# Kernel optimization log

Hardware: AMD Instinct MI355X
Metric: run time of the kernel (lower is better)

Reference implementation:

```python
import jax, jax.numpy as jnp
import numpy as np

N = 50000       # nodes
E = 800000      # edges
D_IN = 128
D_OUT = 128
K = 3           # num_stacks
T = 2           # num_layers


def setup_inputs() -> dict:
    key = jax.random.key(0)
    ks = jax.random.split(key, 10)
    feats = jax.random.normal(ks[0], (N, D_IN), dtype=jnp.float32)
    src = jax.random.randint(ks[1], (E,), 0, N, dtype=jnp.int32)
    dst = jax.random.randint(ks[2], (E,), 0, N, dtype=jnp.int32)
    s = 0.05
    w0 = jax.random.normal(ks[3], (K, D_IN, D_OUT), dtype=jnp.float32) * s
    b0 = jax.random.normal(ks[4], (K, D_OUT), dtype=jnp.float32) * s
    w = jax.random.normal(ks[5], (K, D_OUT, D_OUT), dtype=jnp.float32) * s
    bw = jax.random.normal(ks[6], (K, D_OUT), dtype=jnp.float32) * s
    v = jax.random.normal(ks[7], (K, D_IN, D_OUT), dtype=jnp.float32) * s
    bv = jax.random.normal(ks[8], (K, D_OUT), dtype=jnp.float32) * s
    return {"feats": feats, "src": src, "dst": dst,
            "w0": w0, "b0": b0, "w": w, "bw": bw, "v": v, "bv": bv}


def _propagate(h, src, dst, norm):
    # symmetric degree-normalized SpMM: D^{-1/2} A D^{-1/2} h
    h = h * norm                                   # [N, d]
    agg = jax.ops.segment_sum(h[src], dst, num_segments=N)  # gather + scatter-add
    return agg * norm


def reference(feats, src, dst, w0, b0, w, bw, v, bv):
    ones = jnp.ones((E,), dtype=feats.dtype)
    deg = jnp.clip(jax.ops.segment_sum(ones, dst, num_segments=N), 1.0)
    norm = (deg ** -0.5)[:, None]                  # [N, 1]

    out = jnp.zeros((N, D_OUT), dtype=feats.dtype)
    for k in range(K):
        h = feats
        for t in range(T):
            h = _propagate(h, src, dst, norm)
            if t == 0:
                h = h @ w0[k] + b0[k]
            else:
                h = h @ w[k] + bw[k]
            h = h + (feats @ v[k] + bv[k])         # dropout is identity (p=0, eval)
            h = jax.nn.relu(h)
        out = out + h
    return out / K
```

## Files before the change

kernel.cpp:

```cpp
#include <hip/hip_runtime.h>

#define N_NODES 50000
#define N_EDGES 800000
#define D 128
#define PLANE ((size_t)N_NODES * D)
#define NCHUNK ((N_NODES + 255) / 256)

typedef float f32x4 __attribute__((ext_vector_type(4)));
typedef float f32x2 __attribute__((ext_vector_type(2)));
typedef short bf16x8 __attribute__((ext_vector_type(8)));

__device__ __forceinline__ unsigned short f2bf(float x) {
  unsigned int u = __float_as_uint(x);
  u += 0x7FFFu + ((u >> 16) & 1u);
  return (unsigned short)(u >> 16);
}
__device__ __forceinline__ unsigned char f32_to_fp8(float x) {
  int p = __builtin_amdgcn_cvt_pk_fp8_f32(x, x, 0, false);
  return (unsigned char)(p & 0xFF);
}


__global__ __launch_bounds__(256) void scan_local(const int* __restrict__ cnt,
                                                  int* __restrict__ local,
                                                  int* __restrict__ partial,
                                                  int* __restrict__ bcnt) {
  __shared__ int s[256];
  __shared__ int hist[64];
  int t = threadIdx.x;
  if (t < 64) hist[t] = 0;
  int i = blockIdx.x * 256 + t;
  int v = (i < N_NODES) ? cnt[i] : 0;
  s[t] = v;
  __syncthreads();
  if (i < N_NODES) atomicAdd(&hist[v < 63 ? v : 63], 1);
  for (int off = 1; off < 256; off <<= 1) {
    int tmp = (t >= off) ? s[t - off] : 0;
    __syncthreads();
    s[t] += tmp;
    __syncthreads();
  }
  if (i < N_NODES) local[i] = s[t] - v;
  if (t == 255) partial[blockIdx.x] = s[255];
  if (t < 64) atomicAdd(&bcnt[t], hist[t]);
}

__global__ __launch_bounds__(256) void scan_chunks(const int* __restrict__ partial,
                                                   int* __restrict__ chunk_off,
                                                   int* __restrict__ rowptr,
                                                   const int* __restrict__ bcnt,
                                                   int* __restrict__ gcur) {
  __shared__ int s[256];
  __shared__ int sb[64];
  __shared__ int sbb[64];
  int t = threadIdx.x;
  int v = (t < NCHUNK) ? partial[t] : 0;
  s[t] = v;
  if (t < 64) sb[t] = bcnt[t];
  __syncthreads();
  if (t == 0) {
    int run = 0;
    for (int q = 0; q < 64; ++q) { sbb[q] = run; run += sb[q]; }
  }
  for (int off = 1; off < 256; off <<= 1) {
    int tmp = (t >= off) ? s[t - off] : 0;
    __syncthreads();
    s[t] += tmp;
    __syncthreads();
  }
  if (t < NCHUNK) chunk_off[t] = s[t] - v;
  if (t == 255) rowptr[N_NODES] = s[255];
  if (t < 64) gcur[t] = sbb[t];
}

__global__ __launch_bounds__(256) void finalize_rows(const int* __restrict__ cnt,
                                                     const int* __restrict__ local,
                                                     const int* __restrict__ chunk_off,
                                                     int* __restrict__ rowptr,
                                                     int* __restrict__ cursor,
                                                     float* __restrict__ norm,
                                                     int* __restrict__ gcur,
                                                     int* __restrict__ perm) {
  __shared__ int hcnt[64];
  __shared__ int hbase[64];
  int t = threadIdx.x;
  if (t < 64) hcnt[t] = 0;
  __syncthreads();
  int i = blockIdx.x * 256 + t;
  int b = 0;
  if (i < N_NODES) {
    int r = local[i] + chunk_off[blockIdx.x];
    rowptr[i] = r;
    cursor[i] = r;
    int d = cnt[i];
    b = d < 63 ? d : 63;
    atomicAdd(&hcnt[b], 1);
    if (d < 1) d = 1;
    norm[i] = rsqrtf((float)d);
  }
  __syncthreads();
  if (t < 64) {
    hbase[t] = atomicAdd(&gcur[t], hcnt[t]);
    hcnt[t] = 0;
  }
  __syncthreads();
  if (i < N_NODES) {
    int lp = atomicAdd(&hcnt[b], 1);
    perm[hbase[b] + lp] = i;
  }
}


#define CONV_THREADS ((int)(PLANE / 4))
#define WT_THREADS (2 * 3 * 128 * 256)
#define PREP_TOTAL (CONV_THREADS + WT_THREADS + N_EDGES)

__global__ __launch_bounds__(256) void prep_all(const float* __restrict__ feats,
                                                const float* __restrict__ w0,
                                                const float* __restrict__ w,
                                                const float* __restrict__ v,
                                                const int* __restrict__ dst,
                                                unsigned short* __restrict__ feats_bf,
                                                unsigned short* __restrict__ bt_h1,
                                                unsigned short* __restrict__ bt_out,
                                                int* __restrict__ cnt) {
  int idx = blockIdx.x * 256 + threadIdx.x;
  if (idx < CONV_THREADS) {
    float4 x = ((const float4*)feats)[idx];
    ushort4 o;
    o.x = f2bf(x.x);
    o.y = f2bf(x.y);
    o.z = f2bf(x.z);
    o.w = f2bf(x.w);
    ((ushort4*)feats_bf)[idx] = o;
    return;
  }
  idx -= CONV_THREADS;
  if (idx < WT_THREADS) {
    int buf = idx / 98304;
    int rem = idx - buf * 98304;
    int stack = rem / 32768;
    int rem2 = rem & 32767;
    int n = rem2 >> 8;
    int k = rem2 & 255;
    const float* srcm;
    int kk;
    if (k < 128) {
      srcm = (buf == 0) ? w0 : w;
      kk = k;
    } else {
      srcm = v;
      kk = k - 128;
    }
    float val = srcm[(size_t)stack * 16384 + (size_t)kk * 128 + n];
    unsigned short* dstb = (buf == 0) ? bt_h1 : bt_out;
    dstb[(size_t)stack * 32768 + (size_t)n * 256 + k] = f2bf(val);
    return;
  }
  idx -= WT_THREADS;
  if (idx < N_EDGES) atomicAdd(&cnt[dst[idx]], 1);
}

__global__ __launch_bounds__(256) void csr_fp8(const int* __restrict__ src,
                                               const int* __restrict__ dst,
                                               int* __restrict__ cursor,
                                               int* __restrict__ col,
                                               const float* __restrict__ feats,
                                               const float* __restrict__ norm,
                                               unsigned char* __restrict__ feats_fp8) {
  int idx = blockIdx.x * 256 + threadIdx.x;
  if (idx < CONV_THREADS) {
    float4 x = ((const float4*)feats)[idx];
    float nv = norm[idx >> 5];
    int p = __builtin_amdgcn_cvt_pk_fp8_f32(x.x * nv, x.y * nv, 0, false);
    p = __builtin_amdgcn_cvt_pk_fp8_f32(x.z * nv, x.w * nv, p, true);
    ((int*)feats_fp8)[idx] = p;
    return;
  }
  idx -= CONV_THREADS;
  if (idx < N_EDGES) {
    int pos = atomicAdd(&cursor[dst[idx]], 1);
    col[pos] = src[idx];
  }
}


template <int NK, int STRIDE>
__global__ __launch_bounds__(256) void spmm_rows(const unsigned char* __restrict__ h,
                                                 const float* __restrict__ norm,
                                                 const int* __restrict__ rowptr,
                                                 const int* __restrict__ col,
                                                 const int* __restrict__ perm,
                                                 unsigned short* __restrict__ out) {
  int gi = blockIdx.x * 32 + (threadIdx.x >> 3);
  if (gi >= N_NODES) return;
  int l = threadIdx.x & 7;
  int row = perm[gi];
  int beg = rowptr[row], end = rowptr[row + 1];

  f32x2 acc[NK][8];
#pragma unroll
  for (int m = 0; m < NK; ++m)
#pragma unroll
    for (int j = 0; j < 8; ++j) acc[m][j] = (f32x2)(0.f);

#pragma unroll 2
  for (int e = beg; e < end; ++e) {
    int s = col[e];
    const unsigned char* hp = h + (size_t)s * STRIDE + l * 16;
#pragma unroll
    for (int m = 0; m < NK; ++m) {
      int4 p = *(const int4*)(hp + m * 128);
      acc[m][0] += __builtin_amdgcn_cvt_pk_f32_fp8(p.x, false);
      acc[m][1] += __builtin_amdgcn_cvt_pk_f32_fp8(p.x, true);
      acc[m][2] += __builtin_amdgcn_cvt_pk_f32_fp8(p.y, false);
      acc[m][3] += __builtin_amdgcn_cvt_pk_f32_fp8(p.y, true);
      acc[m][4] += __builtin_amdgcn_cvt_pk_f32_fp8(p.z, false);
      acc[m][5] += __builtin_amdgcn_cvt_pk_f32_fp8(p.z, true);
      acc[m][6] += __builtin_amdgcn_cvt_pk_f32_fp8(p.w, false);
      acc[m][7] += __builtin_amdgcn_cvt_pk_f32_fp8(p.w, true);
    }
  }

  float nd = norm[row];
#pragma unroll
  for (int m = 0; m < NK; ++m) {
    bf16x8 o0, o1;
#pragma unroll
    for (int j = 0; j < 4; ++j) {
      o0[2 * j] = (short)f2bf(acc[m][j].x * nd);
      o0[2 * j + 1] = (short)f2bf(acc[m][j].y * nd);
      o1[2 * j] = (short)f2bf(acc[m][j + 4].x * nd);
      o1[2 * j + 1] = (short)f2bf(acc[m][j + 4].y * nd);
    }
    unsigned short* op = out + (size_t)m * PLANE + (size_t)row * D + l * 16;
    *(bf16x8*)op = o0;
    *(bf16x8*)(op + 8) = o1;
  }
}


__device__ __forceinline__ void stage_B64(unsigned short (*Bs)[256],
                                          const unsigned short* __restrict__ Btg,
                                          int nh, int tid) {
#pragma unroll
  for (int i = 0; i < 8; ++i) {
    int t = tid + i * 256;
    int n = t >> 5;
    int kc = t & 31;
    int kcs = kc ^ (n & 31);
    *(bf16x8*)&Bs[n][kcs * 8] = *(const bf16x8*)(Btg + (size_t)(nh + n) * 256 + kc * 8);
  }
}

__device__ __forceinline__ bf16x8 read_B64(const unsigned short (*Bs)[256], int n,
                                           int chunk) {
  return *(const bf16x8*)&Bs[n][(chunk ^ (n & 31)) * 8];
}

__global__ __launch_bounds__(256) void gemm_h1_fused(
    const unsigned short* __restrict__ P,
    const unsigned short* __restrict__ feats_bf,
    const unsigned short* __restrict__ Bt,
    const float* __restrict__ b0, const float* __restrict__ bv,
    const float* __restrict__ norm,
    unsigned char* __restrict__ h1_fp8) {
  __shared__ unsigned short Bs[64][256];
  int nh = blockIdx.y * 64;

  int tid = threadIdx.x;
  int lane = tid & 63;
  int wv = tid >> 6;
  int ln15 = lane & 15;
  int g = lane >> 4;

  int m0 = blockIdx.x * 128 + wv * 32;
  int r0 = m0 + ln15;
  int r1 = m0 + 16 + ln15;
  if (r0 >= N_NODES) r0 = N_NODES - 1;
  if (r1 >= N_NODES) r1 = N_NODES - 1;

  bf16x8 a0[8], a1[8];
#pragma unroll
  for (int s = 0; s < 4; ++s) {
    a0[s] = *(const bf16x8*)(P + (size_t)r0 * 128 + g * 8 + s * 32);
    a1[s] = *(const bf16x8*)(P + (size_t)r1 * 128 + g * 8 + s * 32);
    a0[s + 4] = *(const bf16x8*)(feats_bf + (size_t)r0 * 128 + g * 8 + s * 32);
    a1[s + 4] = *(const bf16x8*)(feats_bf + (size_t)r1 * 128 + g * 8 + s * 32);
  }

  float nA[4], nB[4];
#pragma unroll
  for (int r = 0; r < 4; ++r) {
    int mA = m0 + g * 4 + r;
    int mB = m0 + 16 + g * 4 + r;
    nA[r] = (mA < N_NODES) ? norm[mA] : 0.f;
    nB[r] = (mB < N_NODES) ? norm[mB] : 0.f;
  }

  for (int stk = 0; stk < 3; ++stk) {
    if (stk) __syncthreads();
    stage_B64(Bs, Bt + (size_t)stk * 32768, nh, tid);
    __syncthreads();

    f32x4 acc0[4], acc1[4];
#pragma unroll
    for (int nt = 0; nt < 4; ++nt) { acc0[nt] = (f32x4)(0.f); acc1[nt] = (f32x4)(0.f); }

#pragma unroll
    for (int s = 0; s < 8; ++s) {
#pragma unroll
      for (int nt = 0; nt < 4; ++nt) {
        bf16x8 bfr = read_B64(Bs, nt * 16 + ln15, s * 4 + g);
        acc0[nt] = __builtin_amdgcn_mfma_f32_16x16x32_bf16(a0[s], bfr, acc0[nt], 0, 0, 0);
        acc1[nt] = __builtin_amdgcn_mfma_f32_16x16x32_bf16(a1[s], bfr, acc1[nt], 0, 0, 0);
      }
    }

#pragma unroll
    for (int nt = 0; nt < 4; ++nt) {
      int colj = nh + nt * 16 + ln15;
      float bsum = b0[stk * 128 + colj] + bv[stk * 128 + colj];
#pragma unroll
      for (int r = 0; r < 4; ++r) {
        int mA = m0 + g * 4 + r;
        int mB = m0 + 16 + g * 4 + r;
        if (mA < N_NODES) {
          float x = acc0[nt][r] + bsum;
          x = x > 0.f ? x : 0.f;
          h1_fp8[(size_t)mA * 384 + stk * 128 + colj] = f32_to_fp8(x * nA[r]);
        }
        if (mB < N_NODES) {
          float x = acc1[nt][r] + bsum;
          x = x > 0.f ? x : 0.f;
          h1_fp8[(size_t)mB * 384 + stk * 128 + colj] = f32_to_fp8(x * nB[r]);
        }
      }
    }
  }
}

__global__ __launch_bounds__(256) void gemm_out_fused(
    const unsigned short* __restrict__ agg,
    const unsigned short* __restrict__ feats_bf,
    const unsigned short* __restrict__ Bt,
    const float* __restrict__ bwp, const float* __restrict__ bvp,
    float* __restrict__ outp) {
  __shared__ unsigned short Bs[64][256];
  int nh = blockIdx.y * 64;

  int tid = threadIdx.x;
  int lane = tid & 63;
  int wv = tid >> 6;
  int ln15 = lane & 15;
  int g = lane >> 4;

  int m0 = blockIdx.x * 128 + wv * 32;
  int r0 = m0 + ln15;
  int r1 = m0 + 16 + ln15;
  if (r0 >= N_NODES) r0 = N_NODES - 1;
  if (r1 >= N_NODES) r1 = N_NODES - 1;

  bf16x8 f0[4], f1[4];
#pragma unroll
  for (int s = 0; s < 4; ++s) {
    f0[s] = *(const bf16x8*)(feats_bf + (size_t)r0 * 128 + g * 8 + s * 32);
    f1[s] = *(const bf16x8*)(feats_bf + (size_t)r1 * 128 + g * 8 + s * 32);
  }

  f32x4 sum0[4], sum1[4];
#pragma unroll
  for (int nt = 0; nt < 4; ++nt) { sum0[nt] = (f32x4)(0.f); sum1[nt] = (f32x4)(0.f); }

  for (int stk = 0; stk < 3; ++stk) {
    if (stk) __syncthreads();
    stage_B64(Bs, Bt + (size_t)stk * 32768, nh, tid);
    __syncthreads();

    const unsigned short* A1 = agg + (size_t)stk * PLANE;
    bf16x8 g0[4], g1[4];
#pragma unroll
    for (int s = 0; s < 4; ++s) {
      g0[s] = *(const bf16x8*)(A1 + (size_t)r0 * 128 + g * 8 + s * 32);
      g1[s] = *(const bf16x8*)(A1 + (size_t)r1 * 128 + g * 8 + s * 32);
    }

    f32x4 acc0[4], acc1[4];
#pragma unroll
    for (int nt = 0; nt < 4; ++nt) { acc0[nt] = (f32x4)(0.f); acc1[nt] = (f32x4)(0.f); }

#pragma unroll
    for (int s = 0; s < 8; ++s) {
      bf16x8 af0 = (s < 4) ? g0[s & 3] : f0[s & 3];
      bf16x8 af1 = (s < 4) ? g1[s & 3] : f1[s & 3];
#pragma unroll
      for (int nt = 0; nt < 4; ++nt) {
        bf16x8 bfr = read_B64(Bs, nt * 16 + ln15, s * 4 + g);
        acc0[nt] = __builtin_amdgcn_mfma_f32_16x16x32_bf16(af0, bfr, acc0[nt], 0, 0, 0);
        acc1[nt] = __builtin_amdgcn_mfma_f32_16x16x32_bf16(af1, bfr, acc1[nt], 0, 0, 0);
      }
    }

#pragma unroll
    for (int nt = 0; nt < 4; ++nt) {
      int colj = nh + nt * 16 + ln15;
      float bsum = bwp[stk * 128 + colj] + bvp[stk * 128 + colj];
#pragma unroll
      for (int r = 0; r < 4; ++r) {
        float x0 = acc0[nt][r] + bsum;
        float x1 = acc1[nt][r] + bsum;
        sum0[nt][r] += (x0 > 0.f ? x0 : 0.f);
        sum1[nt][r] += (x1 > 0.f ? x1 : 0.f);
      }
    }
  }

  const float sc = 1.0f / 3.0f;
#pragma unroll
  for (int nt = 0; nt < 4; ++nt) {
    int colj = nh + nt * 16 + ln15;
#pragma unroll
    for (int r = 0; r < 4; ++r) {
      int mA = m0 + g * 4 + r;
      int mB = m0 + 16 + g * 4 + r;
      if (mA < N_NODES) outp[(size_t)mA * 128 + colj] = sum0[nt][r] * sc;
      if (mB < N_NODES) outp[(size_t)mB * 128 + colj] = sum1[nt][r] * sc;
    }
  }
}


extern "C" void kernel_launch(void* const* d_in, const int* in_sizes, int n_in,
                              void* d_out, int out_size, void* d_ws, size_t ws_size,
                              hipStream_t stream) {
  const float* feats = (const float*)d_in[0];
  const int* src = (const int*)d_in[1];
  const int* dst = (const int*)d_in[2];
  const float* w0 = (const float*)d_in[3];
  const float* b0 = (const float*)d_in[4];
  const float* w = (const float*)d_in[5];
  const float* bw = (const float*)d_in[6];
  const float* v = (const float*)d_in[7];
  const float* bv = (const float*)d_in[8];
  float* out = (float*)d_out;

  char* ws = (char*)d_ws;
  size_t off = 0;
  auto alloc = [&](size_t bytes) {
    void* p = ws + off;
    off += (bytes + 255) & ~(size_t)255;
    return p;
  };
  int* cnt = (int*)alloc((N_NODES + 128) * 4);
  int* bcnt = cnt + N_NODES;
  int* gcur = bcnt + 64;
  int* local = (int*)alloc(N_NODES * 4);
  int* partial = (int*)alloc(NCHUNK * 4);
  int* chunk_off = (int*)alloc(NCHUNK * 4);
  float* norm = (float*)alloc(N_NODES * 4);
  int* rowptr = (int*)alloc((N_NODES + 1) * 4);
  int* cursor = (int*)alloc(N_NODES * 4);
  int* col = (int*)alloc(N_EDGES * 4);
  int* perm = (int*)alloc(N_NODES * 4);
  unsigned short* bt_h1 = (unsigned short*)alloc(3 * 32768 * 2);
  unsigned short* bt_out = (unsigned short*)alloc(3 * 32768 * 2);

  size_t pb = PLANE * 2;
  unsigned short* feats_bf = (unsigned short*)alloc(pb);
  unsigned char* feats_fp8 = (unsigned char*)alloc(PLANE);
  unsigned short* P_bf = (unsigned short*)alloc(pb);
  unsigned char* h1_fp8 = (unsigned char*)alloc(3 * PLANE);
  unsigned short* agg_bf = (unsigned short*)alloc(3 * pb);

  hipMemsetAsync(cnt, 0, (N_NODES + 128) * 4, stream);

  dim3 blk(256);
  prep_all<<<(PREP_TOTAL + 255) / 256, blk, 0, stream>>>(feats, w0, w, v, dst, feats_bf,
                                                         bt_h1, bt_out, cnt);
  scan_local<<<NCHUNK, blk, 0, stream>>>(cnt, local, partial, bcnt);
  scan_chunks<<<1, blk, 0, stream>>>(partial, chunk_off, rowptr, bcnt, gcur);
  finalize_rows<<<NCHUNK, blk, 0, stream>>>(cnt, local, chunk_off, rowptr, cursor, norm,
                                            gcur, perm);
  csr_fp8<<<(CONV_THREADS + N_EDGES + 255) / 256, blk, 0, stream>>>(
      src, dst, cursor, col, feats, norm, feats_fp8);

  int sblocks = (N_NODES + 31) / 32;
  int mblocks = (N_NODES + 127) / 128;
  dim3 ggrid(mblocks, 2);

  spmm_rows<1, 128><<<sblocks, blk, 0, stream>>>(feats_fp8, norm, rowptr, col, perm, P_bf);
  gemm_h1_fused<<<ggrid, blk, 0, stream>>>(P_bf, feats_bf, bt_h1, b0, bv, norm, h1_fp8);
  spmm_rows<3, 384><<<sblocks, blk, 0, stream>>>(h1_fp8, norm, rowptr, col, perm, agg_bf);
  gemm_out_fused<<<ggrid, blk, 0, stream>>>(agg_bf, feats_bf, bt_out, bw, bv, out);
}
```

Baseline: 342.5 us.

## Sort CSR columns into source-index bands per row for gather locality

```diff
diff --git a/kernel.cpp b/kernel.cpp
--- a/kernel.cpp
+++ b/kernel.cpp
@@ -4,7 +4,11 @@
 #define N_EDGES 800000
 #define D 128
 #define PLANE ((size_t)N_NODES * D)
-#define NCHUNK ((N_NODES + 255) / 256)
+#define NBAND 16
+#define BANDW 3125
+#define NB2 (N_NODES * NBAND)
+#define NCHUNK2 (NB2 / 256)
+#define NROWBLK ((N_NODES + 255) / 256)
 
 typedef float f32x4 __attribute__((ext_vector_type(4)));
 typedef float f32x2 __attribute__((ext_vector_type(2)));
@@ -19,84 +23,116 @@
   int p = __builtin_amdgcn_cvt_pk_fp8_f32(x, x, 0, false);
   return (unsigned char)(p & 0xFF);
 }
-
-
-__global__ __launch_bounds__(256) void scan_local(const int* __restrict__ cnt,
-                                                  int* __restrict__ local,
-                                                  int* __restrict__ partial,
-                                                  int* __restrict__ bcnt) {
+__device__ __forceinline__ int band_of(int s) { return (int)((unsigned)s / (unsigned)BANDW); }
+
+
+__global__ __launch_bounds__(256) void scan_local2(const int* __restrict__ cnt2,
+                                                   int* __restrict__ local2,
+                                                   int* __restrict__ partial,
+                                                   int* __restrict__ bcnt) {
   __shared__ int s[256];
   __shared__ int hist[64];
   int t = threadIdx.x;
+  if (blockIdx.x < NCHUNK2) {
+    int i = blockIdx.x * 256 + t;
+    int v = cnt2[i];
+    s[t] = v;
+    __syncthreads();
+    for (int off = 1; off < 256; off <<= 1) {
+      int tmp = (t >= off) ? s[t - off] : 0;
+      __syncthreads();
+      s[t] += tmp;
+      __syncthreads();
+    }
+    local2[i] = s[t] - v;
+    if (t == 255) partial[blockIdx.x] = s[255];
+    return;
+  }
   if (t < 64) hist[t] = 0;
-  int i = blockIdx.x * 256 + t;
-  int v = (i < N_NODES) ? cnt[i] : 0;
-  s[t] = v;
   __syncthreads();
-  if (i < N_NODES) atomicAdd(&hist[v < 63 ? v : 63], 1);
+  int i = (blockIdx.x - NCHUNK2) * 256 + t;
+  if (i < N_NODES) {
+    const int* c = cnt2 + i * NBAND;
+    int d = 0;
+#pragma unroll
+    for (int q = 0; q < NBAND; ++q) d += c[q];
+    atomicAdd(&hist[d < 63 ? d : 63], 1);
+  }
+  __syncthreads();
+  if (t < 64 && hist[t]) atomicAdd(&bcnt[t], hist[t]);
+}
+
+__global__ __launch_bounds__(256) void scan_chunks2(const int* __restrict__ partial,
+                                                    int* __restrict__ chunk_off,
+                                                    int* __restrict__ rowptr2_last,
+                                                    const int* __restrict__ bcnt,
+                                                    int* __restrict__ gcur) {
+  __shared__ int s[256];
+  const int PER = (NCHUNK2 + 255) / 256;
+  int t = threadIdx.x;
+  int loc[PER];
+  int run = 0;
+#pragma unroll
+  for (int j = 0; j < PER; ++j) {
+    int idx = t * PER + j;
+    int v = (idx < NCHUNK2) ? partial[idx] : 0;
+    loc[j] = run;
+    run += v;
+  }
+  s[t] = run;
+  __syncthreads();
   for (int off = 1; off < 256; off <<= 1) {
     int tmp = (t >= off) ? s[t - off] : 0;
     __syncthreads();
     s[t] += tmp;
     __syncthreads();
   }
-  if (i < N_NODES) local[i] = s[t] - v;
-  if (t == 255) partial[blockIdx.x] = s[255];
-  if (t < 64) atomicAdd(&bcnt[t], hist[t]);
-}
-
-__global__ __launch_bounds__(256) void scan_chunks(const int* __restrict__ partial,
-                                                   int* __restrict__ chunk_off,
-                                                   int* __restrict__ rowptr,
-                                                   const int* __restrict__ bcnt,
-                                                   int* __restrict__ gcur) {
-  __shared__ int s[256];
-  __shared__ int sb[64];
-  __shared__ int sbb[64];
-  int t = threadIdx.x;
-  int v = (t < NCHUNK) ? partial[t] : 0;
-  s[t] = v;
-  if (t < 64) sb[t] = bcnt[t];
-  __syncthreads();
+  int base = s[t] - run;
+#pragma unroll
+  for (int j = 0; j < PER; ++j) {
+    int idx = t * PER + j;
+    if (idx < NCHUNK2) chunk_off[idx] = base + loc[j];
+  }
+  if (t == 255) rowptr2_last[0] = s[255];
   if (t == 0) {
-    int run = 0;
-    for (int q = 0; q < 64; ++q) { sbb[q] = run; run += sb[q]; }
-  }
-  for (int off = 1; off < 256; off <<= 1) {
-    int tmp = (t >= off) ? s[t - off] : 0;
-    __syncthreads();
-    s[t] += tmp;
-    __syncthreads();
-  }
-  if (t < NCHUNK) chunk_off[t] = s[t] - v;
-  if (t == 255) rowptr[N_NODES] = s[255];
-  if (t < 64) gcur[t] = sbb[t];
-}
-
-__global__ __launch_bounds__(256) void finalize_rows(const int* __restrict__ cnt,
-                                                     const int* __restrict__ local,
-                                                     const int* __restrict__ chunk_off,
-                                                     int* __restrict__ rowptr,
-                                                     int* __restrict__ cursor,
-                                                     float* __restrict__ norm,
-                                                     int* __restrict__ gcur,
-                                                     int* __restrict__ perm) {
+    int r2 = 0;
+    for (int q = 0; q < 64; ++q) {
+      gcur[q] = r2;
+      r2 += bcnt[q];
+    }
+  }
+}
+
+__global__ __launch_bounds__(256) void finalize2(const int* __restrict__ local2,
+                                                 const int* __restrict__ chunk_off,
+                                                 const int* __restrict__ cnt2,
+                                                 int* __restrict__ rowptr2,
+                                                 int* __restrict__ cursor2,
+                                                 float* __restrict__ norm,
+                                                 int* __restrict__ gcur,
+                                                 int* __restrict__ perm) {
   __shared__ int hcnt[64];
   __shared__ int hbase[64];
   int t = threadIdx.x;
+  if (blockIdx.x < NCHUNK2) {
+    int i = blockIdx.x * 256 + t;
+    int r = local2[i] + chunk_off[blockIdx.x];
+    rowptr2[i] = r;
+    cursor2[i] = r;
+    return;
+  }
   if (t < 64) hcnt[t] = 0;
   __syncthreads();
-  int i = blockIdx.x * 256 + t;
+  int i = (blockIdx.x - NCHUNK2) * 256 + t;
   int b = 0;
   if (i < N_NODES) {
-    int r = local[i] + chunk_off[blockIdx.x];
-    rowptr[i] = r;
-    cursor[i] = r;
-    int d = cnt[i];
+    const int* c = cnt2 + i * NBAND;
+    int d = 0;
+#pragma unroll
+    for (int q = 0; q < NBAND; ++q) d += c[q];
     b = d < 63 ? d : 63;
     atomicAdd(&hcnt[b], 1);
-    if (d < 1) d = 1;
-    norm[i] = rsqrtf((float)d);
+    norm[i] = rsqrtf((float)(d < 1 ? 1 : d));
   }
   __syncthreads();
   if (t < 64) {
@@ -119,11 +155,12 @@
                                                 const float* __restrict__ w0,
                                                 const float* __restrict__ w,
                                                 const float* __restrict__ v,
+                                                const int* __restrict__ src,
                                                 const int* __restrict__ dst,
                                                 unsigned short* __restrict__ feats_bf,
                                                 unsigned short* __restrict__ bt_h1,
                                                 unsigned short* __restrict__ bt_out,
-                                                int* __restrict__ cnt) {
+                                                int* __restrict__ cnt2) {
   int idx = blockIdx.x * 256 + threadIdx.x;
   if (idx < CONV_THREADS) {
     float4 x = ((const float4*)feats)[idx];
@@ -158,12 +195,16 @@
     return;
   }
   idx -= WT_THREADS;
-  if (idx < N_EDGES) atomicAdd(&cnt[dst[idx]], 1);
+  if (idx < N_EDGES) {
+    int dd = dst[idx];
+    int ss = src[idx];
+    atomicAdd(&cnt2[dd * NBAND + band_of(ss)], 1);
+  }
 }
 
 __global__ __launch_bounds__(256) void csr_fp8(const int* __restrict__ src,
                                                const int* __restrict__ dst,
-                                               int* __restrict__ cursor,
+                                               int* __restrict__ cursor2,
                                                int* __restrict__ col,
                                                const float* __restrict__ feats,
                                                const float* __restrict__ norm,
@@ -179,8 +220,10 @@
   }
   idx -= CONV_THREADS;
   if (idx < N_EDGES) {
-    int pos = atomicAdd(&cursor[dst[idx]], 1);
-    col[pos] = src[idx];
+    int dd = dst[idx];
+    int ss = src[idx];
+    int pos = atomicAdd(&cursor2[dd * NBAND + band_of(ss)], 1);
+    col[pos] = ss;
   }
 }
 
@@ -188,7 +231,7 @@
 template <int NK, int STRIDE>
 __global__ __launch_bounds__(256) void spmm_rows(const unsigned char* __restrict__ h,
                                                  const float* __restrict__ norm,
-                                                 const int* __restrict__ rowptr,
+                                                 const int* __restrict__ rowptr2,
                                                  const int* __restrict__ col,
                                                  const int* __restrict__ perm,
                                                  unsigned short* __restrict__ out) {
@@ -196,7 +239,9 @@
   if (gi >= N_NODES) return;
   int l = threadIdx.x & 7;
   int row = perm[gi];
-  int beg = rowptr[row], end = rowptr[row + 1];
+  int beg = rowptr2[row * NBAND];
+  int end = rowptr2[row * NBAND + NBAND];
+  int d = end - beg;
 
   f32x2 acc[NK][8];
 #pragma unroll
@@ -204,21 +249,24 @@
 #pragma unroll
     for (int j = 0; j < 8; ++j) acc[m][j] = (f32x2)(0.f);
 
-#pragma unroll 2
-  for (int e = beg; e < end; ++e) {
-    int s = col[e];
-    const unsigned char* hp = h + (size_t)s * STRIDE + l * 16;
-#pragma unroll
-    for (int m = 0; m < NK; ++m) {
-      int4 p = *(const int4*)(hp + m * 128);
-      acc[m][0] += __builtin_amdgcn_cvt_pk_f32_fp8(p.x, false);
-      acc[m][1] += __builtin_amdgcn_cvt_pk_f32_fp8(p.x, true);
-      acc[m][2] += __builtin_amdgcn_cvt_pk_f32_fp8(p.y, false);
-      acc[m][3] += __builtin_amdgcn_cvt_pk_f32_fp8(p.y, true);
-      acc[m][4] += __builtin_amdgcn_cvt_pk_f32_fp8(p.z, false);
-      acc[m][5] += __builtin_amdgcn_cvt_pk_f32_fp8(p.z, true);
-      acc[m][6] += __builtin_amdgcn_cvt_pk_f32_fp8(p.w, false);
-      acc[m][7] += __builtin_amdgcn_cvt_pk_f32_fp8(p.w, true);
+  for (int ss = 0; ss < NBAND; ++ss) {
+    int e0 = beg + ((ss * d) >> 4);
+    int e1 = beg + (((ss + 1) * d) >> 4);
+    for (int e = e0; e < e1; ++e) {
+      int s = col[e];
+      const unsigned char* hp = h + (size_t)s * STRIDE + l * 16;
+#pragma unroll
+      for (int m = 0; m < NK; ++m) {
+        int4 p = *(const int4*)(hp + m * 128);
+        acc[m][0] += __builtin_amdgcn_cvt_pk_f32_fp8(p.x, false);
+        acc[m][1] += __builtin_amdgcn_cvt_pk_f32_fp8(p.x, true);
+        acc[m][2] += __builtin_amdgcn_cvt_pk_f32_fp8(p.y, false);
+        acc[m][3] += __builtin_amdgcn_cvt_pk_f32_fp8(p.y, true);
+        acc[m][4] += __builtin_amdgcn_cvt_pk_f32_fp8(p.z, false);
+        acc[m][5] += __builtin_amdgcn_cvt_pk_f32_fp8(p.z, true);
+        acc[m][6] += __builtin_amdgcn_cvt_pk_f32_fp8(p.w, false);
+        acc[m][7] += __builtin_amdgcn_cvt_pk_f32_fp8(p.w, true);
+      }
     }
   }
 
@@ -451,15 +499,15 @@
     off += (bytes + 255) & ~(size_t)255;
     return p;
   };
-  int* cnt = (int*)alloc((N_NODES + 128) * 4);
-  int* bcnt = cnt + N_NODES;
+  int* cnt2 = (int*)alloc((NB2 + 128) * 4);
+  int* bcnt = cnt2 + NB2;
   int* gcur = bcnt + 64;
-  int* local = (int*)alloc(N_NODES * 4);
-  int* partial = (int*)alloc(NCHUNK * 4);
-  int* chunk_off = (int*)alloc(NCHUNK * 4);
+  int* local2 = (int*)alloc(NB2 * 4);
+  int* partial = (int*)alloc(NCHUNK2 * 4);
+  int* chunk_off = (int*)alloc(NCHUNK2 * 4);
   float* norm = (float*)alloc(N_NODES * 4);
-  int* rowptr = (int*)alloc((N_NODES + 1) * 4);
-  int* cursor = (int*)alloc(N_NODES * 4);
+  int* rowptr2 = (int*)alloc((NB2 + 1) * 4);
+  int* cursor2 = (int*)alloc(NB2 * 4);
   int* col = (int*)alloc(N_EDGES * 4);
   int* perm = (int*)alloc(N_NODES * 4);
   unsigned short* bt_h1 = (unsigned short*)alloc(3 * 32768 * 2);
@@ -472,24 +520,24 @@
   unsigned char* h1_fp8 = (unsigned char*)alloc(3 * PLANE);
   unsigned short* agg_bf = (unsigned short*)alloc(3 * pb);
 
-  hipMemsetAsync(cnt, 0, (N_NODES + 128) * 4, stream);
+  hipMemsetAsync(cnt2, 0, (NB2 + 128) * 4, stream);
 
   dim3 blk(256);
-  prep_all<<<(PREP_TOTAL + 255) / 256, blk, 0, stream>>>(feats, w0, w, v, dst, feats_bf,
-                                                         bt_h1, bt_out, cnt);
-  scan_local<<<NCHUNK, blk, 0, stream>>>(cnt, local, partial, bcnt);
-  scan_chunks<<<1, blk, 0, stream>>>(partial, chunk_off, rowptr, bcnt, gcur);
-  finalize_rows<<<NCHUNK, blk, 0, stream>>>(cnt, local, chunk_off, rowptr, cursor, norm,
-                                            gcur, perm);
+  prep_all<<<(PREP_TOTAL + 255) / 256, blk, 0, stream>>>(feats, w0, w, v, src, dst,
+                                                         feats_bf, bt_h1, bt_out, cnt2);
+  scan_local2<<<NCHUNK2 + NROWBLK, blk, 0, stream>>>(cnt2, local2, partial, bcnt);
+  scan_chunks2<<<1, blk, 0, stream>>>(partial, chunk_off, rowptr2 + NB2, bcnt, gcur);
+  finalize2<<<NCHUNK2 + NROWBLK, blk, 0, stream>>>(local2, chunk_off, cnt2, rowptr2,
+                                                   cursor2, norm, gcur, perm);
   csr_fp8<<<(CONV_THREADS + N_EDGES + 255) / 256, blk, 0, stream>>>(
-      src, dst, cursor, col, feats, norm, feats_fp8);
+      src, dst, cursor2, col, feats, norm, feats_fp8);
 
   int sblocks = (N_NODES + 31) / 32;
   int mblocks = (N_NODES + 127) / 128;
   dim3 ggrid(mblocks, 2);
 
-  spmm_rows<1, 128><<<sblocks, blk, 0, stream>>>(feats_fp8, norm, rowptr, col, perm, P_bf);
+  spmm_rows<1, 128><<<sblocks, blk, 0, stream>>>(feats_fp8, norm, rowptr2, col, perm, P_bf);
   gemm_h1_fused<<<ggrid, blk, 0, stream>>>(P_bf, feats_bf, bt_h1, b0, bv, norm, h1_fp8);
-  spmm_rows<3, 384><<<sblocks, blk, 0, stream>>>(h1_fp8, norm, rowptr, col, perm, agg_bf);
+  spmm_rows<3, 384><<<sblocks, blk, 0, stream>>>(h1_fp8, norm, rowptr2, col, perm, agg_bf);
   gemm_out_fused<<<ggrid, blk, 0, stream>>>(agg_bf, feats_bf, bt_out, bw, bv, out);
 }
```

Result: no change. 346.0 us (+1.0%).
